# Optimization experiments

Hardware: AMD Instinct MI355X
Metric: run time of the kernel (lower is better)

Reference implementation:

```python
import jax, jax.numpy as jnp
import numpy as np

B, N, H = 4, 4096, 1024
NH, HD, M = 16, 64, 256
EPS = 1e-5


def gaussian_orthogonal(m, d, rng):
    # scaling=0: rows are orthogonal blocks scaled by norms of fresh gaussian rows
    blocks = []
    n_blocks = (m + d - 1) // d
    for _ in range(n_blocks):
        q, _ = np.linalg.qr(rng.standard_normal((d, d)))
        blocks.append(q.T)
    mat = np.concatenate(blocks, 0)[:m]
    multiplier = np.linalg.norm(rng.standard_normal((m, d)), axis=1)
    return (multiplier[:, None] * mat).astype(np.float32)


def setup_inputs():
    key = jax.random.key(0)
    keys = iter(jax.random.split(key, 24))
    rng = np.random.default_rng(0)

    def w(din, dout):
        return jax.random.normal(next(keys), (din, dout), jnp.float32) * 0.02

    inp = {
        'x': jax.random.normal(next(keys), (B, N, H), jnp.float32),
        'enc_outputs': jax.random.normal(next(keys), (B, N, H), jnp.float32),
    }
    for p in ('sa', 'ca'):
        for q in ('wq', 'wk', 'wv', 'wo'):
            inp[f'{p}_{q}'] = w(H, H)
            inp[f'{p}_b{q[1]}'] = jnp.zeros((H,), jnp.float32)
        inp[f'{p}_proj'] = jnp.asarray(gaussian_orthogonal(M, HD, rng))
    inp['ff_w1'] = w(H, 4 * H); inp['ff_b1'] = jnp.zeros((4 * H,), jnp.float32)
    inp['ff_w2'] = w(4 * H, H); inp['ff_b2'] = jnp.zeros((H,), jnp.float32)
    for i in (1, 2, 3):
        inp[f'ln{i}_g'] = jnp.ones((H,), jnp.float32)
        inp[f'ln{i}_b'] = jnp.zeros((H,), jnp.float32)
    return inp


def _split(t):
    b, n, _ = t.shape
    return t.reshape(b, n, NH, HD).transpose(0, 2, 1, 3)  # [b,h,n,d]


def _feat(data, proj):
    # FAVOR+ nonnegative softmax kernel features
    dn = HD ** -0.25
    dd = jnp.einsum('bhnd,md->bhnm', data * dn, proj)
    diag = 0.5 * (dn ** 2) * jnp.sum(data * data, -1)  # [b,h,n]
    dd = dd - diag[..., None] - jnp.max(dd, axis=-1, keepdims=True)
    return (M ** -0.5) * (jnp.exp(dd) + 1e-4)


def _attn(q, k, v, wq, bq, wk, bk, wv, bv, wo, bo, proj):
    b, n, _ = q.shape
    Q = _split(q @ wq + bq)
    K = _split(k @ wk + bk)
    V = _split(v @ wv + bv)
    Qp = _feat(Q, proj)  # [b,h,n,m]
    Kp = _feat(K, proj)
    denom = jnp.einsum('bhnm,bhm->bhn', Qp, Kp.sum(2))[..., None]
    ctx = jnp.einsum('bhnm,bhnd->bhmd', Kp, V)          # O(N) linear attention
    out = jnp.einsum('bhnm,bhmd->bhnd', Qp, ctx) / denom
    # faithful to torch .view(B,-1,hidden) WITHOUT head transpose-back
    out = out.reshape(b, -1, H)
    return out @ wo + bo


def _ln(x, g, b):
    mu = jnp.mean(x, -1, keepdims=True)
    var = jnp.mean((x - mu) ** 2, -1, keepdims=True)
    return (x - mu) / jnp.sqrt(var + EPS) * g + b


def reference(x, enc_outputs, sa_wq, sa_bq, sa_wk, sa_bk, sa_wv, sa_bv, sa_wo, sa_bo,
              sa_proj, ca_wq, ca_bq, ca_wk, ca_bk, ca_wv, ca_bv, ca_wo, ca_bo, ca_proj,
              ff_w1, ff_b1, ff_w2, ff_b2, ln1_g, ln1_b, ln2_g, ln2_b, ln3_g, ln3_b):
    h = _ln(x + _attn(x, x, x, sa_wq, sa_bq, sa_wk, sa_bk, sa_wv, sa_bv, sa_wo, sa_bo, sa_proj), ln1_g, ln1_b)
    h = _ln(h + _attn(h, enc_outputs, enc_outputs, ca_wq, ca_bq, ca_wk, ca_bk, ca_wv, ca_bv, ca_wo, ca_bo, ca_proj), ln2_g, ln2_b)
    ff = jax.nn.gelu(h @ ff_w1 + ff_b1, approximate=True) @ ff_w2 + ff_b2  # dropout prob 0 -> identity
    return _ln(h + ff, ln3_g, ln3_b)
```

## Files before the change

kernel.cpp:

```cpp
#include <hip/hip_runtime.h>
#include <hip/hip_bf16.h>

#define B_ 4
#define N_ 4096
#define H_ 1024
#define NH_ 16
#define HD_ 64
#define M_ 256

typedef __attribute__((ext_vector_type(8))) __bf16 bf16x8;
typedef __attribute__((ext_vector_type(4))) float f32x4;
typedef __attribute__((ext_vector_type(4))) unsigned int u32x4;

__device__ __forceinline__ float bf2f(unsigned short u) {
  union { unsigned int i; float f; } x; x.i = ((unsigned int)u) << 16; return x.f;
}
__device__ __forceinline__ unsigned short f2b(float f) {
  __hip_bfloat16 h = __float2bfloat16(f);
  return *(unsigned short*)&h;
}
__device__ __forceinline__ float gelu_f(float x) {
  const float c = 0.7978845608028654f;
  float t = tanhf(c * (x + 0.044715f * x * x * x));
  return 0.5f * x * (1.0f + t);
}
__device__ __forceinline__ bf16x8 ones8() {
  union { unsigned int u[4]; bf16x8 v; } o;
  o.u[0] = 0x3F803F80u; o.u[1] = 0x3F803F80u; o.u[2] = 0x3F803F80u; o.u[3] = 0x3F803F80u;
  return o.v;
}

typedef __attribute__((address_space(3))) unsigned int as3_uint;
typedef const __attribute__((address_space(1))) unsigned int as1_uint;
__device__ __forceinline__ void gload16(const void* g, void* l) {
  __builtin_amdgcn_global_load_lds((as1_uint*)g, (as3_uint*)l, 16, 0, 0);
}

template<int ACT>
__launch_bounds__(256)
__global__ void gemm_mfma(const unsigned short* __restrict__ A, int lda,
                          const unsigned short* __restrict__ BT,
                          const float* __restrict__ bias,
                          unsigned short* __restrict__ C, int ldc, int K) {
  __shared__ __align__(16) char LDS[65536];

  const int tid = threadIdx.x;
  const int nwg = gridDim.x * gridDim.y;
  const int lin = blockIdx.y * gridDim.x + blockIdx.x;
  const int mm = (lin & 7) * (nwg >> 3) + (lin >> 3);
  const int bx = mm % gridDim.x, by = mm / gridDim.x;
  const int row0 = by * 128;
  const int col0 = bx * 128;

  const int w = tid >> 6, lane = tid & 63;
  const int wm = w >> 1, wn = w & 1;
  const int ln = lane & 15, hi = lane >> 4;
  const int rswz = (ln & 7) << 4;

  const int srow = w * 8 + (lane >> 3);
  const int schunk = ((lane & 7) ^ (lane >> 3)) * 8;
  const unsigned short* Ag = A + (long long)(row0 + srow) * lda + schunk;
  const unsigned short* Bg = BT + (long long)(col0 + srow) * K + schunk;
  const int ldsw = w * 1024;

  f32x4 acc[4][4];
#pragma unroll
  for (int i = 0; i < 4; ++i)
#pragma unroll
    for (int j = 0; j < 4; ++j) acc[i][j] = (f32x4){0.f, 0.f, 0.f, 0.f};

  auto STAGE = [&](int p, int k0) {
    char* dst = LDS + p * 32768 + ldsw;
#pragma unroll
    for (int i = 0; i < 4; ++i) {
      gload16(Ag + (long long)i * 32 * lda + k0, dst + i * 4096);
      gload16(Bg + (long long)i * 32 * K + k0, dst + 16384 + i * 4096);
    }
  };
  auto COMPUTE = [&](int p) {
    char* AsB = LDS + p * 32768;
    char* BsB = AsB + 16384;
#pragma unroll
    for (int kc = 0; kc < 2; ++kc) {
      const int koff = (kc * 64 + hi * 16) ^ rswz;
      bf16x8 av[4], bv[4];
#pragma unroll
      for (int i = 0; i < 4; ++i)
        av[i] = *(bf16x8*)(AsB + (wm * 64 + i * 16 + ln) * 128 + koff);
#pragma unroll
      for (int j = 0; j < 4; ++j)
        bv[j] = *(bf16x8*)(BsB + (wn * 64 + j * 16 + ln) * 128 + koff);
      __builtin_amdgcn_s_setprio(1);
#pragma unroll
      for (int i = 0; i < 4; ++i)
#pragma unroll
        for (int j = 0; j < 4; ++j)
          acc[i][j] = __builtin_amdgcn_mfma_f32_16x16x32_bf16(av[i], bv[j], acc[i][j], 0, 0, 0);
      __builtin_amdgcn_s_setprio(0);
    }
  };

  const int nT = K >> 6;
  STAGE(0, 0);
  int cur = 0;
  for (int t = 0; t < nT; ++t) {
    if (t + 1 < nT) {
      STAGE(cur ^ 1, (t + 1) * 64);
      asm volatile("s_waitcnt vmcnt(8)" ::: "memory");
    } else {
      asm volatile("s_waitcnt vmcnt(0)" ::: "memory");
    }
    __builtin_amdgcn_sched_barrier(0);
    __builtin_amdgcn_s_barrier();
    COMPUTE(cur);
    __builtin_amdgcn_s_barrier();
    cur ^= 1;
  }

  char* SB = LDS;
#pragma unroll
  for (int j = 0; j < 4; ++j) {
    const int lcol = wn * 64 + j * 16 + ln;
    const float bj = bias ? bias[col0 + lcol] : 0.0f;
#pragma unroll
    for (int i = 0; i < 4; ++i) {
      const int rb_ = wm * 64 + i * 16 + hi * 4;
#pragma unroll
      for (int r = 0; r < 4; ++r) {
        float v = acc[i][j][r] + bj;
        if (ACT == 1) v = gelu_f(v);
        const int row = rb_ + r;
        *(unsigned short*)(SB + ((row * 256 + lcol * 2) ^ ((row & 7) << 4))) = f2b(v);
      }
    }
  }
  __syncthreads();
#pragma unroll
  for (int p = 0; p < 8; ++p) {
    const int idx = p * 256 + tid;
    const int row = idx >> 4, seg = idx & 15;
    u32x4 v = *(u32x4*)(SB + ((row * 256 + seg * 16) ^ ((row & 7) << 4)));
    __builtin_nontemporal_store(v, (u32x4*)(C + (long long)(row0 + row) * ldc + col0 + seg * 8));
  }
}

__launch_bounds__(256)
__global__ void ctxksum_mfma(const unsigned short* __restrict__ QKV,
                             const unsigned short* __restrict__ pjB,
                             float* __restrict__ ksumP,
                             float* __restrict__ ctxP) {
  __shared__ char Kt[2][8192];
  __shared__ char Vt[2][8192];
  __shared__ char Pt[32768];
  __shared__ float rmaxL[4][64];
  __shared__ float ssqL[64];
  const int z = blockIdx.z, b = z >> 4, hh = z & 15;
  const int sp = blockIdx.x;
  const long long n0 = sp * 512;
  const unsigned short* Kg = QKV + (long long)(b * 4096) * 3072 + 1024 + hh * 64;
  const unsigned short* Vg = QKV + (long long)(b * 4096) * 3072 + 2048 + hh * 64;
  const int tid = threadIdx.x;
  const int w = tid >> 6, lane = tid & 63;
  const int ln = lane & 15, hi = lane >> 4;
  const int rswz = (ln & 7) << 4;
  const bf16x8 onesf = ones8();

  f32x4 accC[4][4];
#pragma unroll
  for (int i = 0; i < 4; ++i)
#pragma unroll
    for (int j = 0; j < 4; ++j) accC[i][j] = (f32x4){0.f, 0.f, 0.f, 0.f};
  f32x4 accK[4];
#pragma unroll
  for (int i = 0; i < 4; ++i) accK[i] = (f32x4){0.f, 0.f, 0.f, 0.f};

  const int vn = tid >> 2, vd0 = (tid & 3) * 16;
  ushort4 vr[4];
  auto VLOAD = [&](long long nt) {
    const unsigned short* src = Vg + (nt + vn) * 3072 + vd0;
    vr[0] = *(const ushort4*)src;
    vr[1] = *(const ushort4*)(src + 4);
    vr[2] = *(const ushort4*)(src + 8);
    vr[3] = *(const ushort4*)(src + 12);
  };
  auto VWRITE = [&](int buf) {
    unsigned short vals[16] = {vr[0].x, vr[0].y, vr[0].z, vr[0].w,
                               vr[1].x, vr[1].y, vr[1].z, vr[1].w,
                               vr[2].x, vr[2].y, vr[2].z, vr[2].w,
                               vr[3].x, vr[3].y, vr[3].z, vr[3].w};
#pragma unroll
    for (int e = 0; e < 16; ++e) {
      int d = vd0 + e;
      *(unsigned short*)(Vt[buf] + ((d * 128 + vn * 2) ^ ((d & 7) << 4))) = vals[e];
    }
  };
  auto KSTAGE = [&](long long nt, int buf) {
#pragma unroll
    for (int p = 0; p < 2; ++p) {
      int id = p * 256 + tid;
      int r = id >> 3, c = id & 7;
      gload16(Kg + (nt + r) * 3072 + ((c ^ (r & 7)) * 8), Kt[buf] + id * 16);
    }
  };

  KSTAGE(n0, 0);
  VLOAD(n0);
  VWRITE(0);
  __syncthreads();

  for (int t = 0; t < 8; ++t) {
    const int cur = t & 1;
    if (t < 7) {
      KSTAGE(n0 + (t + 1) * 64, cur ^ 1);
      VLOAD(n0 + (t + 1) * 64);
    }

    f32x4 accT[4][4];
#pragma unroll
    for (int i = 0; i < 4; ++i)
#pragma unroll
      for (int j = 0; j < 4; ++j) accT[i][j] = (f32x4){0.f, 0.f, 0.f, 0.f};
#pragma unroll
    for (int kc = 0; kc < 2; ++kc) {
      const int koff = (kc * 64 + hi * 16) ^ rswz;
      bf16x8 kv[4], bq[4];
#pragma unroll
      for (int nj = 0; nj < 4; ++nj)
        kv[nj] = *(bf16x8*)(Kt[cur] + (nj * 16 + ln) * 128 + koff);
#pragma unroll
      for (int mi = 0; mi < 4; ++mi)
        bq[mi] = *(const bf16x8*)(pjB + (w * 64 + mi * 16 + ln) * 64 + kc * 32 + hi * 8);
      __builtin_amdgcn_s_setprio(1);
#pragma unroll
      for (int mi = 0; mi < 4; ++mi)
#pragma unroll
        for (int nj = 0; nj < 4; ++nj)
          accT[mi][nj] = __builtin_amdgcn_mfma_f32_16x16x32_bf16(bq[mi], kv[nj], accT[mi][nj], 0, 0, 0);
      __builtin_amdgcn_s_setprio(0);
    }

#pragma unroll
    for (int nj = 0; nj < 4; ++nj) {
      float mx = accT[0][nj][0];
#pragma unroll
      for (int mi = 0; mi < 4; ++mi)
#pragma unroll
        for (int r = 0; r < 4; ++r) mx = fmaxf(mx, accT[mi][nj][r]);
      mx = fmaxf(mx, __shfl_xor(mx, 16, 64));
      mx = fmaxf(mx, __shfl_xor(mx, 32, 64));
      if (hi == 0) rmaxL[w][nj * 16 + ln] = mx;
    }
    {
      int r = tid >> 2, q = tid & 3;
      int b0 = (r * 128 + q * 32) ^ ((r & 7) << 4);
      int b1 = (r * 128 + q * 32 + 16) ^ ((r & 7) << 4);
      u32x4 x0 = *(u32x4*)(Kt[cur] + b0);
      u32x4 x1 = *(u32x4*)(Kt[cur] + b1);
      float s = 0.f;
#pragma unroll
      for (int e = 0; e < 4; ++e) {
        float a0 = bf2f((unsigned short)(x0[e] & 0xffff)), a1 = bf2f((unsigned short)(x0[e] >> 16));
        float a2 = bf2f((unsigned short)(x1[e] & 0xffff)), a3 = bf2f((unsigned short)(x1[e] >> 16));
        s += a0 * a0 + a1 * a1 + a2 * a2 + a3 * a3;
      }
      s += __shfl_xor(s, 1, 64);
      s += __shfl_xor(s, 2, 64);
      if (q == 0) ssqL[r] = s;
    }
    __syncthreads();

    float base[4];
#pragma unroll
    for (int nj = 0; nj < 4; ++nj) {
      int n = nj * 16 + ln;
      base[nj] = 0.0625f * ssqL[n] +
                 fmaxf(fmaxf(rmaxL[0][n], rmaxL[1][n]), fmaxf(rmaxL[2][n], rmaxL[3][n]));
    }
#pragma unroll
    for (int mi = 0; mi < 4; ++mi)
#pragma unroll
      for (int nj = 0; nj < 4; ++nj)
#pragma unroll
        for (int r = 0; r < 4; ++r) {
          float v = 0.0625f * (expf(accT[mi][nj][r] - base[nj]) + 1e-4f);
          int m = w * 64 + mi * 16 + hi * 4 + r;
          int n = nj * 16 + ln;
          *(unsigned short*)(Pt + ((m * 128 + n * 2) ^ ((m & 7) << 4))) = f2b(v);
        }
    if (t < 7) VWRITE(cur ^ 1);
    __syncthreads();

#pragma unroll
    for (int kc = 0; kc < 2; ++kc) {
      const int koff = (kc * 64 + hi * 16) ^ rswz;
      bf16x8 am[4], bv[4];
#pragma unroll
      for (int i = 0; i < 4; ++i)
        am[i] = *(bf16x8*)(Pt + (w * 64 + i * 16 + ln) * 128 + koff);
#pragma unroll
      for (int j = 0; j < 4; ++j)
        bv[j] = *(bf16x8*)(Vt[cur] + (j * 16 + ln) * 128 + koff);
      __builtin_amdgcn_s_setprio(1);
#pragma unroll
      for (int i = 0; i < 4; ++i)
#pragma unroll
        for (int j = 0; j < 4; ++j)
          accC[i][j] = __builtin_amdgcn_mfma_f32_16x16x32_bf16(am[i], bv[j], accC[i][j], 0, 0, 0);
#pragma unroll
      for (int i = 0; i < 4; ++i)
        accK[i] = __builtin_amdgcn_mfma_f32_16x16x32_bf16(am[i], onesf, accK[i], 0, 0, 0);
      __builtin_amdgcn_s_setprio(0);
    }
  }

  if (ln == 0) {
#pragma unroll
    for (int mi = 0; mi < 4; ++mi)
#pragma unroll
      for (int r = 0; r < 4; ++r)
        ksumP[((long long)z * 8 + sp) * 256 + w * 64 + mi * 16 + hi * 4 + r] = accK[mi][r];
  }

  float* ctxPs = ctxP + ((long long)z * 8 + sp) * 16384;
#pragma unroll
  for (int dh = 0; dh < 2; ++dh) {
    __syncthreads();
#pragma unroll
    for (int i = 0; i < 4; ++i)
#pragma unroll
      for (int jj = 0; jj < 2; ++jj) {
        int j = dh * 2 + jj;
#pragma unroll
        for (int r = 0; r < 4; ++r) {
          int m = w * 64 + i * 16 + hi * 4 + r;
          int dl = jj * 16 + ln;
          *(float*)(Pt + ((m * 128 + dl * 4) ^ ((m & 7) << 4))) = accC[i][j][r];
        }
      }
    __syncthreads();
#pragma unroll
    for (int p = 0; p < 8; ++p) {
      int idx = p * 256 + tid;
      int row = idx >> 3, seg = idx & 7;
      u32x4 v = *(u32x4*)(Pt + ((row * 128 + seg * 16) ^ ((row & 7) << 4)));
      __builtin_nontemporal_store(v, (u32x4*)(ctxPs + dh * 8192 + row * 32 + seg * 4));
    }
  }
}

__launch_bounds__(256)
__global__ void ctx_fin(const float* __restrict__ ctxP, const float* __restrict__ ksumP,
                        unsigned short* __restrict__ ctxbf, float* __restrict__ ksumF) {
  __shared__ float acc[16384];
  const int z = blockIdx.x;
  const int tid = threadIdx.x;
  const float* base = ctxP + (long long)z * 8 * 16384;
  for (int i = tid; i < 16384; i += 256) {
    float s = 0.f;
#pragma unroll
    for (int q = 0; q < 8; ++q) s += base[(long long)q * 16384 + i];
    acc[i] = s;
  }
  {
    const float* kb = ksumP + (long long)z * 8 * 256;
    float s = 0.f;
#pragma unroll
    for (int q = 0; q < 8; ++q) s += kb[q * 256 + tid];
    ksumF[z * 256 + tid] = s;
  }
  __syncthreads();
  unsigned short* dst = ctxbf + (long long)z * 16384;
  for (int cc = tid; cc < 2048; cc += 256) {
    int mh = cc >> 10, rem = cc & 1023, d = rem >> 4, cl = rem & 15;
    int m0 = mh * 128 + cl * 8;
    int dh = d >> 5, dl = d & 31;
    ushort4 o0, o1;
    o0.x = f2b(acc[dh * 8192 + (m0 + 0) * 32 + dl]);
    o0.y = f2b(acc[dh * 8192 + (m0 + 1) * 32 + dl]);
    o0.z = f2b(acc[dh * 8192 + (m0 + 2) * 32 + dl]);
    o0.w = f2b(acc[dh * 8192 + (m0 + 3) * 32 + dl]);
    o1.x = f2b(acc[dh * 8192 + (m0 + 4) * 32 + dl]);
    o1.y = f2b(acc[dh * 8192 + (m0 + 5) * 32 + dl]);
    o1.z = f2b(acc[dh * 8192 + (m0 + 6) * 32 + dl]);
    o1.w = f2b(acc[dh * 8192 + (m0 + 7) * 32 + dl]);
    unsigned short* p = dst + (long long)mh * 8192 + (d * 16 + (cl ^ (d & 7))) * 8;
    *(ushort4*)p = o0;
    *(ushort4*)(p + 4) = o1;
  }
}

__launch_bounds__(256)
__global__ void ao_fused(const unsigned short* __restrict__ QKV,
                         const unsigned short* __restrict__ pjB,
                         const float* __restrict__ ksum,
                         const unsigned short* __restrict__ ctxbf,
                         unsigned short* __restrict__ AO) {
  __shared__ char Qt[8192];
  __shared__ char Ps[32768];
  __shared__ char Ch[32768];
  __shared__ float rmaxL[4][64];
  __shared__ float ssqL[64];
  __shared__ float dprt[4][64];
  __shared__ float denomS[64];
  __shared__ float ksL[256];
  const int z = blockIdx.z, b = z >> 4, hh = z & 15;
  const int n0 = blockIdx.x * 64;
  const unsigned short* Qg = QKV + (long long)(b * 4096) * 3072 + hh * 64;
  const int tid = threadIdx.x;
  const int w = tid >> 6, lane = tid & 63;
  const int ln = lane & 15, hi = lane >> 4;
  const int rswz = (ln & 7) << 4;

#pragma unroll
  for (int p = 0; p < 8; ++p) {
    int id = p * 256 + tid;
    gload16(ctxbf + (long long)z * 16384 + id * 8, Ch + id * 16);
  }
#pragma unroll
  for (int p = 0; p < 2; ++p) {
    int id = p * 256 + tid;
    int r = id >> 3, c = id & 7;
    gload16(Qg + (long long)(n0 + r) * 3072 + ((c ^ (r & 7)) * 8), Qt + id * 16);
  }
  ksL[tid] = ksum[z * 256 + tid];
  __syncthreads();

  f32x4 accT[4][4];
#pragma unroll
  for (int i = 0; i < 4; ++i)
#pragma unroll
    for (int j = 0; j < 4; ++j) accT[i][j] = (f32x4){0.f, 0.f, 0.f, 0.f};
#pragma unroll
  for (int kc = 0; kc < 2; ++kc) {
    const int koff = (kc * 64 + hi * 16) ^ rswz;
    bf16x8 qv[4], bq[4];
#pragma unroll
    for (int nj = 0; nj < 4; ++nj)
      qv[nj] = *(bf16x8*)(Qt + (nj * 16 + ln) * 128 + koff);
#pragma unroll
    for (int mi = 0; mi < 4; ++mi)
      bq[mi] = *(const bf16x8*)(pjB + (w * 64 + mi * 16 + ln) * 64 + kc * 32 + hi * 8);
    __builtin_amdgcn_s_setprio(1);
#pragma unroll
    for (int mi = 0; mi < 4; ++mi)
#pragma unroll
      for (int nj = 0; nj < 4; ++nj)
        accT[mi][nj] = __builtin_amdgcn_mfma_f32_16x16x32_bf16(bq[mi], qv[nj], accT[mi][nj], 0, 0, 0);
    __builtin_amdgcn_s_setprio(0);
  }

#pragma unroll
  for (int nj = 0; nj < 4; ++nj) {
    float mx = accT[0][nj][0];
#pragma unroll
    for (int mi = 0; mi < 4; ++mi)
#pragma unroll
      for (int r = 0; r < 4; ++r) mx = fmaxf(mx, accT[mi][nj][r]);
    mx = fmaxf(mx, __shfl_xor(mx, 16, 64));
    mx = fmaxf(mx, __shfl_xor(mx, 32, 64));
    if (hi == 0) rmaxL[w][nj * 16 + ln] = mx;
  }
  {
    int r = tid >> 2, q = tid & 3;
    int b0 = (r * 128 + q * 32) ^ ((r & 7) << 4);
    int b1 = (r * 128 + q * 32 + 16) ^ ((r & 7) << 4);
    u32x4 x0 = *(u32x4*)(Qt + b0);
    u32x4 x1 = *(u32x4*)(Qt + b1);
    float s = 0.f;
#pragma unroll
    for (int e = 0; e < 4; ++e) {
      float a0 = bf2f((unsigned short)(x0[e] & 0xffff)), a1 = bf2f((unsigned short)(x0[e] >> 16));
      float a2 = bf2f((unsigned short)(x1[e] & 0xffff)), a3 = bf2f((unsigned short)(x1[e] >> 16));
      s += a0 * a0 + a1 * a1 + a2 * a2 + a3 * a3;
    }
    s += __shfl_xor(s, 1, 64);
    s += __shfl_xor(s, 2, 64);
    if (q == 0) ssqL[r] = s;
  }
  __syncthreads();

  float base[4];
#pragma unroll
  for (int nj = 0; nj < 4; ++nj) {
    int n = nj * 16 + ln;
    base[nj] = 0.0625f * ssqL[n] +
               fmaxf(fmaxf(rmaxL[0][n], rmaxL[1][n]), fmaxf(rmaxL[2][n], rmaxL[3][n]));
  }
  float ksv[4][4];
#pragma unroll
  for (int mi = 0; mi < 4; ++mi)
#pragma unroll
    for (int r = 0; r < 4; ++r)
      ksv[mi][r] = ksL[w * 64 + mi * 16 + hi * 4 + r];
  float dp[4] = {0.f, 0.f, 0.f, 0.f};
#pragma unroll
  for (int mi = 0; mi < 4; ++mi)
#pragma unroll
    for (int nj = 0; nj < 4; ++nj)
#pragma unroll
      for (int r = 0; r < 4; ++r) {
        float v = 0.0625f * (expf(accT[mi][nj][r] - base[nj]) + 1e-4f);
        unsigned short vb = f2b(v);
        int m = w * 64 + mi * 16 + hi * 4 + r;
        int n = nj * 16 + ln;
        *(unsigned short*)(Ps + n * 512 + ((m * 2) ^ ((n & 7) << 4))) = vb;
        dp[nj] += bf2f(vb) * ksv[mi][r];
      }
#pragma unroll
  for (int nj = 0; nj < 4; ++nj) {
    dp[nj] += __shfl_xor(dp[nj], 16, 64);
    dp[nj] += __shfl_xor(dp[nj], 32, 64);
    if (hi == 0) dprt[w][nj * 16 + ln] = dp[nj];
  }
  __syncthreads();
  if (tid < 64) denomS[tid] = dprt[0][tid] + dprt[1][tid] + dprt[2][tid] + dprt[3][tid];

  f32x4 accO[4];
#pragma unroll
  for (int j = 0; j < 4; ++j) accO[j] = (f32x4){0.f, 0.f, 0.f, 0.f};
#pragma unroll
  for (int mh = 0; mh < 2; ++mh) {
#pragma unroll
    for (int ms = 0; ms < 4; ++ms) {
      const int koff = (ms * 64 + hi * 16);
      bf16x8 ap = *(bf16x8*)(Ps + (w * 16 + ln) * 512 + ((mh * 256 + koff) ^ rswz));
      bf16x8 bc[4];
#pragma unroll
      for (int j = 0; j < 4; ++j)
        bc[j] = *(bf16x8*)(Ch + mh * 16384 + (j * 16 + ln) * 256 + (koff ^ rswz));
      __builtin_amdgcn_s_setprio(1);
#pragma unroll
      for (int j = 0; j < 4; ++j)
        accO[j] = __builtin_amdgcn_mfma_f32_16x16x32_bf16(ap, bc[j], accO[j], 0, 0, 0);
      __builtin_amdgcn_s_setprio(0);
    }
  }
  __syncthreads();

  float inv[4];
#pragma unroll
  for (int r = 0; r < 4; ++r) inv[r] = 1.0f / denomS[w * 16 + hi * 4 + r];
  char* Ct = Qt;
#pragma unroll
  for (int j = 0; j < 4; ++j)
#pragma unroll
    for (int r = 0; r < 4; ++r) {
      int n = w * 16 + hi * 4 + r;
      int d = j * 16 + ln;
      *(unsigned short*)(Ct + ((n * 128 + d * 2) ^ ((n & 7) << 4))) = f2b(accO[j][r] * inv[r]);
    }
  __syncthreads();
#pragma unroll
  for (int p = 0; p < 2; ++p) {
    int idx = p * 256 + tid;
    int row = idx >> 3, seg = idx & 7;
    u32x4 v = *(u32x4*)(Ct + ((row * 128 + seg * 16) ^ ((row & 7) << 4)));
    *(u32x4*)(AO + (long long)(b * 4096 + n0 + row) * 1024 + hh * 64 + seg * 8) = v;
  }
}

__launch_bounds__(256)
__global__ void wt_cvt(const float* __restrict__ in, unsigned short* __restrict__ out,
                       int K, int N) {
  __shared__ float t[32][33];
  int k0 = blockIdx.y * 32, n0 = blockIdx.x * 32;
  int tx = threadIdx.x & 31, ty = threadIdx.x >> 5;
  for (int r = ty; r < 32; r += 8) t[r][tx] = in[(long long)(k0 + r) * N + n0 + tx];
  __syncthreads();
  for (int r = ty; r < 32; r += 8) out[(long long)(n0 + r) * K + k0 + tx] = f2b(t[tx][r]);
}

__launch_bounds__(256)
__global__ void wt_cvt4(const float* __restrict__ w0, const float* __restrict__ w1,
                        const float* __restrict__ w2, const float* __restrict__ w3,
                        unsigned short* __restrict__ out) {
  __shared__ float t[32][33];
  const float* in = (blockIdx.z == 0) ? w0 : (blockIdx.z == 1) ? w1
                    : (blockIdx.z == 2) ? w2 : w3;
  unsigned short* o = out + (long long)blockIdx.z * 1048576;
  int k0 = blockIdx.y * 32, n0 = blockIdx.x * 32;
  int tx = threadIdx.x & 31, ty = threadIdx.x >> 5;
  for (int r = ty; r < 32; r += 8) t[r][tx] = in[(long long)(k0 + r) * H_ + n0 + tx];
  __syncthreads();
  for (int r = ty; r < 32; r += 8) o[(long long)(n0 + r) * H_ + k0 + tx] = f2b(t[tx][r]);
}

__launch_bounds__(256)
__global__ void projB_cvt2(const float* __restrict__ pj_sa, const float* __restrict__ pj_ca,
                           unsigned short* __restrict__ out) {
  int i = blockIdx.x * 256 + threadIdx.x;
  const float* src = (i < 16384) ? pj_sa : pj_ca;
  out[i] = f2b(0.35355339059327373f * src[i & 16383]);
}

__launch_bounds__(256)
__global__ void bias_cat(const float* __restrict__ b0, const float* __restrict__ b1,
                         const float* __restrict__ b2, float* __restrict__ out) {
  int i = blockIdx.x * 256 + threadIdx.x;
  float v;
  if (i < 1024) v = b0[i];
  else if (i < 2048) v = b1[i - 1024];
  else v = b2[i - 2048];
  out[i] = v;
}

__launch_bounds__(256)
__global__ void cvt_bf16(const float* __restrict__ in, unsigned short* __restrict__ out,
                         long long n) {
  long long stride = (long long)gridDim.x * 1024;
  for (long long i = ((long long)blockIdx.x * 256 + threadIdx.x) * 4; i < n; i += stride) {
    float4 v = *(const float4*)&in[i];
    ushort4 o;
    o.x = f2b(v.x); o.y = f2b(v.y); o.z = f2b(v.z); o.w = f2b(v.w);
    *(ushort4*)&out[i] = o;
  }
}

__launch_bounds__(256)
__global__ void ln_k(const float* __restrict__ resf, const unsigned short* __restrict__ resb,
                     const unsigned short* __restrict__ po,
                     const float* __restrict__ g, const float* __restrict__ be,
                     float* __restrict__ outf, unsigned short* __restrict__ outb) {
  long long row = blockIdx.x;
  int t = threadIdx.x;
  float x0, x1, x2, x3;
  if (resf) {
    float4 va = ((const float4*)(resf + row * H_))[t];
    x0 = va.x; x1 = va.y; x2 = va.z; x3 = va.w;
  } else {
    ushort4 va = ((const ushort4*)(resb + row * H_))[t];
    x0 = bf2f(va.x); x1 = bf2f(va.y); x2 = bf2f(va.z); x3 = bf2f(va.w);
  }
  {
    ushort4 vp = ((const ushort4*)(po + row * H_))[t];
    x0 += bf2f(vp.x); x1 += bf2f(vp.y); x2 += bf2f(vp.z); x3 += bf2f(vp.w);
  }
  float s = x0 + x1 + x2 + x3;
  float q = x0 * x0 + x1 * x1 + x2 * x2 + x3 * x3;
#pragma unroll
  for (int m = 1; m < 64; m <<= 1) { s += __shfl_xor(s, m, 64); q += __shfl_xor(q, m, 64); }
  __shared__ float ssum[4], ssq[4];
  int w = t >> 6, lane = t & 63;
  if (lane == 0) { ssum[w] = s; ssq[w] = q; }
  __syncthreads();
  s = ssum[0] + ssum[1] + ssum[2] + ssum[3];
  q = ssq[0] + ssq[1] + ssq[2] + ssq[3];
  float mean = s * (1.0f / H_);
  float var = q * (1.0f / H_) - mean * mean;
  float rstd = rsqrtf(var + 1e-5f);
  float4 vg = ((const float4*)g)[t];
  float4 vbe = ((const float4*)be)[t];
  float o0 = (x0 - mean) * rstd * vg.x + vbe.x;
  float o1 = (x1 - mean) * rstd * vg.y + vbe.y;
  float o2 = (x2 - mean) * rstd * vg.z + vbe.z;
  float o3 = (x3 - mean) * rstd * vg.w + vbe.w;
  if (outf) {
    float4 o; o.x = o0; o.y = o1; o.z = o2; o.w = o3;
    ((float4*)(outf + row * H_))[t] = o;
  }
  if (outb) {
    ushort4 ob; ob.x = f2b(o0); ob.y = f2b(o1); ob.z = f2b(o2); ob.w = f2b(o3);
    ((ushort4*)(outb + row * H_))[t] = ob;
  }
}

extern "C" void kernel_launch(void* const* d_in, const int* in_sizes, int n_in,
                              void* d_out, int out_size, void* d_ws, size_t ws_size,
                              hipStream_t stream) {
  (void)in_sizes; (void)n_in; (void)out_size; (void)ws_size;
  const float* x      = (const float*)d_in[0];
  const float* enc    = (const float*)d_in[1];
  const float* sa_w[4] = {(const float*)d_in[2], (const float*)d_in[4], (const float*)d_in[6], (const float*)d_in[8]};
  const float* sa_b[4] = {(const float*)d_in[3], (const float*)d_in[5], (const float*)d_in[7], (const float*)d_in[9]};
  const float* sa_pj  = (const float*)d_in[10];
  const float* ca_w[4] = {(const float*)d_in[11], (const float*)d_in[13], (const float*)d_in[15], (const float*)d_in[17]};
  const float* ca_b[4] = {(const float*)d_in[12], (const float*)d_in[14], (const float*)d_in[16], (const float*)d_in[18]};
  const float* ca_pj  = (const float*)d_in[19];
  const float* ff_w1  = (const float*)d_in[20];
  const float* ff_b1  = (const float*)d_in[21];
  const float* ff_w2  = (const float*)d_in[22];
  const float* ff_b2  = (const float*)d_in[23];
  const float* ln1_g  = (const float*)d_in[24];
  const float* ln1_b  = (const float*)d_in[25];
  const float* ln2_g  = (const float*)d_in[26];
  const float* ln2_b  = (const float*)d_in[27];
  const float* ln3_g  = (const float*)d_in[28];
  const float* ln3_b  = (const float*)d_in[29];

  float* ws = (float*)d_ws;
  unsigned short* XB = (unsigned short*)(ws);
  unsigned short* EB = (unsigned short*)(ws + 8388608LL);
  unsigned short* QKVb = (unsigned short*)(ws + 16777216LL);
  unsigned short* PO = (unsigned short*)(ws + 41943040LL);
  float* ctxP = ws + 41943040LL;
  unsigned short* MID2 = QKVb;
  unsigned short* FO2 = PO;
  unsigned short* WTph = (unsigned short*)(ws + 52428800LL);
  unsigned short* pjB = (unsigned short*)(ws + 54525952LL);
  float* ksumP = ws + 54542336LL;
  float* ksumF = ws + 54673408LL;
  unsigned short* ctxbf = (unsigned short*)(ws + 55607296LL);
  float* biasC = ws + 56131584LL;

  unsigned short* ff1T = EB;
  unsigned short* ff2T = EB + 4194304LL;
  unsigned short* pjB_sa = pjB, *pjB_ca = pjB + 16384;

  dim3 blk(256, 1, 1);
  const int LDQ = 3072;

  projB_cvt2<<<dim3(128), blk, 0, stream>>>(sa_pj, ca_pj, pjB);
  cvt_bf16<<<dim3(2048), blk, 0, stream>>>(x, XB, 16777216LL);

  auto attn_core = [&](const unsigned short* pj, const float* wo_bias) {
    ctxksum_mfma<<<dim3(8, 1, 64), blk, 0, stream>>>(QKVb, pj, ksumP, ctxP);
    ctx_fin<<<dim3(64), blk, 0, stream>>>(ctxP, ksumP, ctxbf, ksumF);
    ao_fused<<<dim3(64, 1, 64), blk, 0, stream>>>(QKVb, pj, ksumF, ctxbf, EB);
    gemm_mfma<0><<<dim3(8, 128), blk, 0, stream>>>(EB, H_, WTph + 3145728, wo_bias, PO, H_, H_);
  };

  wt_cvt4<<<dim3(32, 32, 4), blk, 0, stream>>>(sa_w[0], sa_w[1], sa_w[2], sa_w[3], WTph);
  bias_cat<<<dim3(12), blk, 0, stream>>>(sa_b[0], sa_b[1], sa_b[2], biasC);
  gemm_mfma<0><<<dim3(24, 128), blk, 0, stream>>>(XB, H_, WTph, biasC, QKVb, LDQ, H_);
  attn_core(pjB_sa, sa_b[3]);
  ln_k<<<dim3(16384), blk, 0, stream>>>(x, nullptr, PO, ln1_g, ln1_b, nullptr, XB);

  cvt_bf16<<<dim3(2048), blk, 0, stream>>>(enc, EB, 16777216LL);
  wt_cvt4<<<dim3(32, 32, 4), blk, 0, stream>>>(ca_w[0], ca_w[1], ca_w[2], ca_w[3], WTph);
  bias_cat<<<dim3(8), blk, 0, stream>>>(ca_b[1], ca_b[2], nullptr, biasC);
  gemm_mfma<0><<<dim3(8, 128), blk, 0, stream>>>(XB, H_, WTph, ca_b[0], QKVb, LDQ, H_);
  gemm_mfma<0><<<dim3(16, 128), blk, 0, stream>>>(EB, H_, WTph + 1048576, biasC, QKVb + 1024, LDQ, H_);
  attn_core(pjB_ca, ca_b[3]);
  ln_k<<<dim3(16384), blk, 0, stream>>>(nullptr, XB, PO, ln2_g, ln2_b, nullptr, XB);

  wt_cvt<<<dim3(128, 32), blk, 0, stream>>>(ff_w1, ff1T, H_, 4096);
  wt_cvt<<<dim3(32, 128), blk, 0, stream>>>(ff_w2, ff2T, 4096, H_);
  for (int c = 0; c < 2; ++c) {
    const long long co = (long long)c * 8192 * H_;
    gemm_mfma<1><<<dim3(32, 64), blk, 0, stream>>>(XB + co, H_, ff1T, ff_b1, MID2, 4096, H_);
    gemm_mfma<0><<<dim3(8, 64), blk, 0, stream>>>(MID2, 4096, ff2T, ff_b2, FO2, H_, 4096);
    ln_k<<<dim3(8192), blk, 0, stream>>>(nullptr, XB + co, FO2, ln3_g, ln3_b,
                                         (float*)d_out + co, nullptr);
  }
}
```

Before: 1.242 ms.

## Replace 128x128 GEMM with 256x256-tile, 512-thread MFMA GEMM kernel

Replaces the 128x128 tile, 256-thread bf16 MFMA GEMM with a 256x256 tile version using 512 threads (8 waves, each computing 128x64) and 128 KB of double-buffered LDS. All GEMM launches (QKV, output projection, FFN) move to the larger tile with correspondingly smaller grids. The aim is higher arithmetic intensity per byte loaded from global memory, which cuts A/B reloads. In exchange, occupancy drops to one workgroup per CU, register pressure rises with 32 accumulators per wave, and grids get smaller (e.g. 256 blocks for the N=1024 GEMMs), which risks poorer latency hiding and tail effects.

New measurement: 1.267 ms. +2.0%, slower.

```diff
diff --git a/kernel.cpp b/kernel.cpp
--- a/kernel.cpp
+++ b/kernel.cpp
@@ -37,62 +37,62 @@
 }
 
 template<int ACT>
-__launch_bounds__(256)
-__global__ void gemm_mfma(const unsigned short* __restrict__ A, int lda,
-                          const unsigned short* __restrict__ BT,
-                          const float* __restrict__ bias,
-                          unsigned short* __restrict__ C, int ldc, int K) {
-  __shared__ __align__(16) char LDS[65536];
+__launch_bounds__(512)
+__global__ void gemm256(const unsigned short* __restrict__ A, int lda,
+                        const unsigned short* __restrict__ BT,
+                        const float* __restrict__ bias,
+                        unsigned short* __restrict__ C, int ldc, int K) {
+  __shared__ __align__(16) char LDS[131072];
 
   const int tid = threadIdx.x;
   const int nwg = gridDim.x * gridDim.y;
   const int lin = blockIdx.y * gridDim.x + blockIdx.x;
   const int mm = (lin & 7) * (nwg >> 3) + (lin >> 3);
   const int bx = mm % gridDim.x, by = mm / gridDim.x;
-  const int row0 = by * 128;
-  const int col0 = bx * 128;
+  const int row0 = by * 256;
+  const int col0 = bx * 256;
 
   const int w = tid >> 6, lane = tid & 63;
-  const int wm = w >> 1, wn = w & 1;
+  const int wm = w >> 2, wn = w & 3;
   const int ln = lane & 15, hi = lane >> 4;
   const int rswz = (ln & 7) << 4;
 
-  const int srow = w * 8 + (lane >> 3);
-  const int schunk = ((lane & 7) ^ (lane >> 3)) * 8;
-  const unsigned short* Ag = A + (long long)(row0 + srow) * lda + schunk;
-  const unsigned short* Bg = BT + (long long)(col0 + srow) * K + schunk;
-  const int ldsw = w * 1024;
-
-  f32x4 acc[4][4];
-#pragma unroll
-  for (int i = 0; i < 4; ++i)
+  const int srow = tid >> 3;
+  const int schunk = ((tid & 7) ^ (srow & 7)) * 8;
+  const unsigned short* Ab = A + (long long)(row0 + srow) * lda + schunk;
+  const unsigned short* Bb = BT + (long long)(col0 + srow) * K + schunk;
+
+  f32x4 acc[8][4];
+#pragma unroll
+  for (int i = 0; i < 8; ++i)
 #pragma unroll
     for (int j = 0; j < 4; ++j) acc[i][j] = (f32x4){0.f, 0.f, 0.f, 0.f};
 
-  auto STAGE = [&](int p, int k0) {
-    char* dst = LDS + p * 32768 + ldsw;
-#pragma unroll
-    for (int i = 0; i < 4; ++i) {
-      gload16(Ag + (long long)i * 32 * lda + k0, dst + i * 4096);
-      gload16(Bg + (long long)i * 32 * K + k0, dst + 16384 + i * 4096);
+  auto STAGE = [&](int buf, int k0) {
+    char* dA = LDS + buf * 65536;
+    char* dB = dA + 32768;
+#pragma unroll
+    for (int p = 0; p < 4; ++p) {
+      gload16(Ab + (long long)p * 64 * lda + k0, dA + p * 8192 + tid * 16);
+      gload16(Bb + (long long)p * 64 * K + k0, dB + p * 8192 + tid * 16);
     }
   };
-  auto COMPUTE = [&](int p) {
-    char* AsB = LDS + p * 32768;
-    char* BsB = AsB + 16384;
+  auto COMPUTE = [&](int buf) {
+    char* AsB = LDS + buf * 65536;
+    char* BsB = AsB + 32768;
 #pragma unroll
     for (int kc = 0; kc < 2; ++kc) {
       const int koff = (kc * 64 + hi * 16) ^ rswz;
-      bf16x8 av[4], bv[4];
-#pragma unroll
-      for (int i = 0; i < 4; ++i)
-        av[i] = *(bf16x8*)(AsB + (wm * 64 + i * 16 + ln) * 128 + koff);
+      bf16x8 av[8], bv[4];
+#pragma unroll
+      for (int i = 0; i < 8; ++i)
+        av[i] = *(bf16x8*)(AsB + (wm * 128 + i * 16 + ln) * 128 + koff);
 #pragma unroll
       for (int j = 0; j < 4; ++j)
         bv[j] = *(bf16x8*)(BsB + (wn * 64 + j * 16 + ln) * 128 + koff);
       __builtin_amdgcn_s_setprio(1);
 #pragma unroll
-      for (int i = 0; i < 4; ++i)
+      for (int i = 0; i < 8; ++i)
 #pragma unroll
         for (int j = 0; j < 4; ++j)
           acc[i][j] = __builtin_amdgcn_mfma_f32_16x16x32_bf16(av[i], bv[j], acc[i][j], 0, 0, 0);
@@ -123,23 +123,23 @@
     const int lcol = wn * 64 + j * 16 + ln;
     const float bj = bias ? bias[col0 + lcol] : 0.0f;
 #pragma unroll
-    for (int i = 0; i < 4; ++i) {
-      const int rb_ = wm * 64 + i * 16 + hi * 4;
+    for (int i = 0; i < 8; ++i) {
+      const int rb_ = wm * 128 + i * 16 + hi * 4;
 #pragma unroll
       for (int r = 0; r < 4; ++r) {
         float v = acc[i][j][r] + bj;
         if (ACT == 1) v = gelu_f(v);
         const int row = rb_ + r;
-        *(unsigned short*)(SB + ((row * 256 + lcol * 2) ^ ((row & 7) << 4))) = f2b(v);
+        *(unsigned short*)(SB + ((row * 512 + lcol * 2) ^ ((row & 7) << 4))) = f2b(v);
       }
     }
   }
   __syncthreads();
 #pragma unroll
-  for (int p = 0; p < 8; ++p) {
-    const int idx = p * 256 + tid;
-    const int row = idx >> 4, seg = idx & 15;
-    u32x4 v = *(u32x4*)(SB + ((row * 256 + seg * 16) ^ ((row & 7) << 4)));
+  for (int p = 0; p < 16; ++p) {
+    const int idx = p * 512 + tid;
+    const int row = idx >> 5, seg = idx & 31;
+    u32x4 v = *(u32x4*)(SB + ((row * 512 + seg * 16) ^ ((row & 7) << 4)));
     __builtin_nontemporal_store(v, (u32x4*)(C + (long long)(row0 + row) * ldc + col0 + seg * 8));
   }
 }
@@ -707,6 +707,7 @@
   unsigned short* pjB_sa = pjB, *pjB_ca = pjB + 16384;
 
   dim3 blk(256, 1, 1);
+  dim3 blk512(512, 1, 1);
   const int LDQ = 3072;
 
   projB_cvt2<<<dim3(128), blk, 0, stream>>>(sa_pj, ca_pj, pjB);
@@ -716,20 +717,20 @@
     ctxksum_mfma<<<dim3(8, 1, 64), blk, 0, stream>>>(QKVb, pj, ksumP, ctxP);
     ctx_fin<<<dim3(64), blk, 0, stream>>>(ctxP, ksumP, ctxbf, ksumF);
     ao_fused<<<dim3(64, 1, 64), blk, 0, stream>>>(QKVb, pj, ksumF, ctxbf, EB);
-    gemm_mfma<0><<<dim3(8, 128), blk, 0, stream>>>(EB, H_, WTph + 3145728, wo_bias, PO, H_, H_);
+    gemm256<0><<<dim3(4, 64), blk512, 0, stream>>>(EB, H_, WTph + 3145728, wo_bias, PO, H_, H_);
   };
 
   wt_cvt4<<<dim3(32, 32, 4), blk, 0, stream>>>(sa_w[0], sa_w[1], sa_w[2], sa_w[3], WTph);
   bias_cat<<<dim3(12), blk, 0, stream>>>(sa_b[0], sa_b[1], sa_b[2], biasC);
-  gemm_mfma<0><<<dim3(24, 128), blk, 0, stream>>>(XB, H_, WTph, biasC, QKVb, LDQ, H_);
+  gemm256<0><<<dim3(12, 64), blk512, 0, stream>>>(XB, H_, WTph, biasC, QKVb, LDQ, H_);
   attn_core(pjB_sa, sa_b[3]);
   ln_k<<<dim3(16384), blk, 0, stream>>>(x, nullptr, PO, ln1_g, ln1_b, nullptr, XB);
 
   cvt_bf16<<<dim3(2048), blk, 0, stream>>>(enc, EB, 16777216LL);
   wt_cvt4<<<dim3(32, 32, 4), blk, 0, stream>>>(ca_w[0], ca_w[1], ca_w[2], ca_w[3], WTph);
   bias_cat<<<dim3(8), blk, 0, stream>>>(ca_b[1], ca_b[2], nullptr, biasC);
-  gemm_mfma<0><<<dim3(8, 128), blk, 0, stream>>>(XB, H_, WTph, ca_b[0], QKVb, LDQ, H_);
-  gemm_mfma<0><<<dim3(16, 128), blk, 0, stream>>>(EB, H_, WTph + 1048576, biasC, QKVb + 1024, LDQ, H_);
+  gemm256<0><<<dim3(4, 64), blk512, 0, stream>>>(XB, H_, WTph, ca_b[0], QKVb, LDQ, H_);
+  gemm256<0><<<dim3(8, 64), blk512, 0, stream>>>(EB, H_, WTph + 1048576, biasC, QKVb + 1024, LDQ, H_);
   attn_core(pjB_ca, ca_b[3]);
   ln_k<<<dim3(16384), blk, 0, stream>>>(nullptr, XB, PO, ln2_g, ln2_b, nullptr, XB);
 
@@ -737,8 +738,8 @@
   wt_cvt<<<dim3(32, 128), blk, 0, stream>>>(ff_w2, ff2T, 4096, H_);
   for (int c = 0; c < 2; ++c) {
     const long long co = (long long)c * 8192 * H_;
-    gemm_mfma<1><<<dim3(32, 64), blk, 0, stream>>>(XB + co, H_, ff1T, ff_b1, MID2, 4096, H_);
-    gemm_mfma<0><<<dim3(8, 64), blk, 0, stream>>>(MID2, 4096, ff2T, ff_b2, FO2, H_, 4096);
+    gemm256<1><<<dim3(16, 32), blk512, 0, stream>>>(XB + co, H_, ff1T, ff_b1, MID2, 4096, H_);
+    gemm256<0><<<dim3(4, 32), blk512, 0, stream>>>(MID2, 4096, ff2T, ff_b2, FO2, H_, 4096);
     ln_k<<<dim3(8192), blk, 0, stream>>>(nullptr, XB + co, FO2, ln3_g, ln3_b,
                                          (float*)d_out + co, nullptr);
   }
```
